# Performance work log

Hardware: AMD Instinct MI355X
Metric: run time of the kernel (lower is better)

Reference implementation:

```python
import jax, jax.numpy as jnp
import numpy as np

N = 100000   # nodes
E = 1600000  # edges
G = 256      # graphs in batch
IN = 128     # in_feats
H = 64       # h_feats


def _xavier(k, shape):
    fan_in, fan_out = shape
    lim = float(np.sqrt(6.0 / (fan_in + fan_out)))
    return jax.random.uniform(k, shape, jnp.float32, -lim, lim)


def setup_inputs() -> dict:
    key = jax.random.key(0)
    ks = jax.random.split(key, 12)
    x = jax.random.normal(ks[0], (N, IN), jnp.float32)
    src = jax.random.randint(ks[1], (E,), 0, N)
    dst = jax.random.randint(ks[2], (E,), 0, N)
    ew = jax.random.uniform(ks[3], (E,), jnp.float32)
    gid = jnp.sort(jax.random.randint(ks[4], (N,), 0, G))
    def lin(k, fi, fo):
        kw, kb = jax.random.split(k)
        lim = float(np.sqrt(1.0 / fi))
        return (jax.random.uniform(kw, (fi, fo), jnp.float32, -lim, lim),
                jax.random.uniform(kb, (fo,), jnp.float32, -lim, lim))
    W1 = _xavier(ks[5], (IN, H)); b1 = jnp.zeros((H,), jnp.float32)
    W2 = _xavier(ks[6], (H, H));  b2 = jnp.zeros((H,), jnp.float32)
    W3 = _xavier(ks[7], (H, H));  b3 = jnp.zeros((H,), jnp.float32)
    Dw1, Db1 = lin(ks[8], H, 16)
    Dw2, Db2 = lin(ks[9], 16, 8)
    Dw3, Db3 = lin(ks[10], 8, 1)
    return {"x": x, "src": src, "dst": dst, "ew": ew, "gid": gid,
            "W1": W1, "b1": b1, "W2": W2, "b2": b2, "W3": W3, "b3": b3,
            "Dw1": Dw1, "Db1": Db1, "Dw2": Dw2, "Db2": Db2, "Dw3": Dw3, "Db3": Db3}


def reference(x, src, dst, ew, gid, W1, b1, W2, b2, W3, b3,
              Dw1, Db1, Dw2, Db2, Dw3, Db3):
    n = x.shape[0]
    # DGL GraphConv norm='both': unweighted degrees, clamped to >= 1
    deg_out = jnp.zeros((n,), x.dtype).at[src].add(1.0)
    deg_in = jnp.zeros((n,), x.dtype).at[dst].add(1.0)
    ns = jax.lax.rsqrt(jnp.maximum(deg_out, 1.0))  # src-side norm
    nd = jax.lax.rsqrt(jnp.maximum(deg_in, 1.0))   # dst-side norm

    def conv(h, W, b):
        # apply weight first (in >= out), then gather-scale-scatter
        h = (h * ns[:, None]) @ W                      # [N, out]
        m = h[src] * ew[:, None]                       # [E, out] edge messages
        agg = jnp.zeros((n, W.shape[1]), h.dtype).at[dst].add(m)
        return agg * nd[:, None] + b

    h = jax.nn.relu(conv(x, W1, b1))
    h = jax.nn.relu(conv(h, W2, b2))
    h = jax.nn.relu(conv(h, W3, b3))

    # mean_nodes: per-graph mean pooling
    counts = jnp.zeros((G,), h.dtype).at[gid].add(1.0)
    pooled = jnp.zeros((G, h.shape[1]), h.dtype).at[gid].add(h)
    pooled = pooled / jnp.maximum(counts, 1.0)[:, None]

    h = jax.nn.relu(pooled @ Dw1 + Db1)
    h = jax.nn.relu(h @ Dw2 + Db2)
    return jax.nn.sigmoid(h @ Dw3 + Db3)  # [G, 1]
```

## Files before the change

### kernel.cpp

```cpp
#include <hip/hip_runtime.h>
#include <math.h>

#define N_NODES 100000
#define N_EDGES 1600000
#define G_GRAPHS 256
#define IN_F 128
#define H_F 64

#define HB 40
#define HCHUNK (N_EDGES / HB)
#define NWORDS (N_NODES / 4)
#define HNODES 25000
#define HWORDS (HNODES / 4)
#define HR 4

#define NREG 160
#define REG_NODES 625
#define BUCKET_CAP 11000
#define BSPAN 6400
#define NB_BUCKET (N_EDGES / BSPAN)

typedef unsigned int uint_t;
typedef unsigned short ushort_t;
typedef unsigned char uchar_t;
typedef __attribute__((ext_vector_type(8))) short short8;
typedef __attribute__((ext_vector_type(4))) float floatx4;
typedef __attribute__((ext_vector_type(2))) float floatx2;

__device__ __forceinline__ ushort_t f2bf(float f) {
  uint_t u = __float_as_uint(f);
  uint_t r = (u + 0x7fffu + ((u >> 16) & 1u)) >> 16;
  return (ushort_t)r;
}
__device__ __forceinline__ float bflo(uint_t u) { return __uint_as_float(u << 16); }
__device__ __forceinline__ uchar_t f2fp8(float f) {
  return (uchar_t)(__builtin_amdgcn_cvt_pk_fp8_f32(f, f, 0, false) & 0xff);
}

__global__ __launch_bounds__(256) void build_a_kernel(
    const int* __restrict__ src, const int* __restrict__ dst,
    const float* __restrict__ ew, int* __restrict__ bcnt,
    uint2* __restrict__ bucket, uint_t* __restrict__ p8src) {
  __shared__ uint_t shm[BSPAN + 2 * NREG];
  if (blockIdx.x < NB_BUCKET) {
    uint_t* rl = shm;
    int* cnt = (int*)(shm + BSPAN);
    int* cur = cnt + NREG;
    const int e0 = blockIdx.x * BSPAN;

    for (int i = threadIdx.x; i < NREG; i += 256) cnt[i] = 0;
    __syncthreads();

    for (int i = threadIdx.x; i < BSPAN; i += 256) {
      uint_t d = (uint_t)dst[e0 + i];
      uint_t r = d / REG_NODES;
      uint_t loc = d - r * REG_NODES;
      rl[i] = (r << 16) | loc;
      atomicAdd(&cnt[r], 1);
    }
    __syncthreads();

    for (int i = threadIdx.x; i < NREG; i += 256)
      cur[i] = atomicAdd(&bcnt[i], cnt[i]);
    __syncthreads();

    for (int i = threadIdx.x; i < BSPAN; i += 256) {
      uint_t v = rl[i];
      uint_t r = v >> 16, loc = v & 0xffffu;
      int pos = atomicAdd(&cur[r], 1);
      if (pos < BUCKET_CAP)
        bucket[(size_t)r * BUCKET_CAP + pos] = make_uint2(
            (loc << 17) | (uint_t)src[e0 + i], __float_as_uint(ew[e0 + i]));
    }
  } else {
    uint_t* h = shm;
    const int idx = blockIdx.x - NB_BUCKET;
    const int r = idx / HB;
    const int b = idx % HB;
    const uint_t rbase = (uint_t)(r * HNODES);

    for (int i = threadIdx.x; i < HWORDS; i += 256) h[i] = 0u;
    __syncthreads();

    const uint4* k4 = (const uint4*)(src + b * HCHUNK);
    for (int i = threadIdx.x; i < HCHUNK / 4; i += 256) {
      uint4 v = k4[i];
      uint_t t;
      t = v.x - rbase; if (t < (uint_t)HNODES) atomicAdd(&h[t >> 2], 1u << ((t & 3u) * 8u));
      t = v.y - rbase; if (t < (uint_t)HNODES) atomicAdd(&h[t >> 2], 1u << ((t & 3u) * 8u));
      t = v.z - rbase; if (t < (uint_t)HNODES) atomicAdd(&h[t >> 2], 1u << ((t & 3u) * 8u));
      t = v.w - rbase; if (t < (uint_t)HNODES) atomicAdd(&h[t >> 2], 1u << ((t & 3u) * 8u));
    }
    __syncthreads();

    uint_t* outp = p8src + (size_t)b * NWORDS + r * HWORDS;
    for (int i = threadIdx.x; i < HWORDS; i += 256) outp[i] = h[i];
  }
}

__global__ __launch_bounds__(256) void build_b_kernel(
    const uint2* __restrict__ bucket, const int* __restrict__ bcnt,
    const uint_t* __restrict__ p8src, uint_t* __restrict__ csr,
    int2* __restrict__ rc, float* __restrict__ nd, float* __restrict__ ns) {
  __shared__ uint_t staged[BUCKET_CAP];
  __shared__ int cnt[REG_NODES];
  __shared__ int sc[REG_NODES];
  __shared__ int ts[256];
  const int tid = threadIdx.x;
  if (blockIdx.x >= NREG) {
    int w = (blockIdx.x - NREG) * 256 + tid;
    if (w >= NWORDS) return;
    int c0 = 0, c1 = 0, c2 = 0, c3 = 0;
    for (int b = 0; b < HB; ++b) {
      uint_t xv = p8src[(size_t)b * NWORDS + w];
      c0 += (int)(xv & 0xffu);
      c1 += (int)((xv >> 8) & 0xffu);
      c2 += (int)((xv >> 16) & 0xffu);
      c3 += (int)((xv >> 24) & 0xffu);
    }
    ((float4*)ns)[w] = make_float4(
        rsqrtf(fmaxf((float)c0, 1.0f)), rsqrtf(fmaxf((float)c1, 1.0f)),
        rsqrtf(fmaxf((float)c2, 1.0f)), rsqrtf(fmaxf((float)c3, 1.0f)));
    return;
  }
  const int r = blockIdx.x;
  const int nE = min(bcnt[r], BUCKET_CAP);

  ts[tid] = (tid < NREG) ? min(bcnt[tid], BUCKET_CAP) : 0;
  for (int i = tid; i < REG_NODES; i += 256) cnt[i] = 0;
  __syncthreads();
  for (int off = 1; off < 256; off <<= 1) {
    int t = (tid >= off) ? ts[tid - off] : 0;
    __syncthreads();
    ts[tid] += t;
    __syncthreads();
  }
  const int csr_base = (r == 0) ? 0 : ts[r - 1];
  __syncthreads();

  const uint2* bk = bucket + (size_t)r * BUCKET_CAP;
  for (int i = tid; i < nE; i += 256) atomicAdd(&cnt[bk[i].x >> 17], 1);
  __syncthreads();

  const int loc0 = tid * 3;
  int c3v[3], s = 0;
#pragma unroll
  for (int k = 0; k < 3; ++k) {
    int idx = loc0 + k;
    c3v[k] = (idx < REG_NODES) ? cnt[idx] : 0;
    s += c3v[k];
  }
  __syncthreads();
  ts[tid] = s;
  __syncthreads();
  for (int off = 1; off < 256; off <<= 1) {
    int t = (tid >= off) ? ts[tid - off] : 0;
    __syncthreads();
    ts[tid] += t;
    __syncthreads();
  }
  int run = (tid == 0) ? 0 : ts[tid - 1];
#pragma unroll
  for (int k = 0; k < 3; ++k) {
    int idx = loc0 + k;
    if (idx < REG_NODES) {
      sc[idx] = run;
      int v = r * REG_NODES + idx;
      rc[v] = make_int2(csr_base + run, c3v[k]);
      nd[v] = rsqrtf(fmaxf((float)c3v[k], 1.0f));
      run += c3v[k];
    }
  }
  __syncthreads();

  for (int i = tid; i < nE; i += 256) {
    uint2 e = bk[i];
    uint_t loc = e.x >> 17;
    int pos = atomicAdd(&sc[loc], 1);
    staged[pos] = ((uint_t)(f2bf(__uint_as_float(e.y)) & 0x7fff) << 17) |
                  (e.x & 0x1ffffu);
  }
  __syncthreads();

  for (int i = tid; i < nE; i += 256) csr[csr_base + i] = staged[i];
}

template <int K, bool AFP32>
__global__ __launch_bounds__(256) void gemm_mfma_kernel(
    const void* __restrict__ Xin, const float* __restrict__ W,
    const float* __restrict__ ns, uchar_t* __restrict__ T, int ntiles) {
  constexpr int CH = K / 32;
  constexpr int WROW = K + 8;
  __shared__ __align__(16) ushort_t Wt[64 * WROW];
  const int tid = threadIdx.x;

  for (int i = tid; i < K * 64; i += 256) {
    int k = i >> 6, nn = i & 63;
    Wt[nn * WROW + k] = f2bf(W[i]);
  }
  __syncthreads();

  const int wave = tid >> 6;
  const int lane = tid & 63;
  const int tile = blockIdx.x * 4 + wave;
  if (tile >= ntiles) return;
  const int m = lane & 15;
  const int q = lane >> 4;
  const int node0 = tile * 16;

  short8 afrag[CH];
  if (AFP32) {
    const float* xr = (const float*)Xin + (size_t)(node0 + m) * K + q * 8;
#pragma unroll
    for (int c = 0; c < CH; ++c) {
      float4 xa = *(const float4*)(xr + c * 32);
      float4 xb = *(const float4*)(xr + c * 32 + 4);
      short8 a;
      a[0] = (short)f2bf(xa.x); a[1] = (short)f2bf(xa.y);
      a[2] = (short)f2bf(xa.z); a[3] = (short)f2bf(xa.w);
      a[4] = (short)f2bf(xb.x); a[5] = (short)f2bf(xb.y);
      a[6] = (short)f2bf(xb.z); a[7] = (short)f2bf(xb.w);
      afrag[c] = a;
    }
  } else {
    const ushort_t* xr = (const ushort_t*)Xin + (size_t)(node0 + m) * K + q * 8;
#pragma unroll
    for (int c = 0; c < CH; ++c)
      afrag[c] = *(const short8*)(xr + c * 32);
  }

  floatx4 acc[4];
#pragma unroll
  for (int t = 0; t < 4; ++t) acc[t] = (floatx4){0.f, 0.f, 0.f, 0.f};

#pragma unroll
  for (int t = 0; t < 4; ++t) {
    const ushort_t* wr = &Wt[(t * 16 + m) * WROW + q * 8];
#pragma unroll
    for (int c = 0; c < CH; ++c) {
      short8 bfrag = *(const short8*)(wr + c * 32);
      acc[t] = __builtin_amdgcn_mfma_f32_16x16x32_bf16(afrag[c], bfrag, acc[t], 0, 0, 0);
    }
  }

  float4 nsv = *(const float4*)(ns + node0 + q * 4);
  const float nsa[4] = {nsv.x, nsv.y, nsv.z, nsv.w};
#pragma unroll
  for (int t = 0; t < 4; ++t) {
#pragma unroll
    for (int r = 0; r < 4; ++r) {
      int node = node0 + q * 4 + r;
      T[(size_t)node * 64 + t * 16 + m] = f2fp8(acc[t][r] * nsa[r]);
    }
  }
}

#define GACC(p, w)                                                   \
  a = __builtin_amdgcn_cvt_pk_f32_fp8((p).x, false);                 \
  acc[0] = fmaf(a.x, (w), acc[0]); acc[1] = fmaf(a.y, (w), acc[1]);  \
  a = __builtin_amdgcn_cvt_pk_f32_fp8((p).x, true);                  \
  acc[2] = fmaf(a.x, (w), acc[2]); acc[3] = fmaf(a.y, (w), acc[3]);  \
  a = __builtin_amdgcn_cvt_pk_f32_fp8((p).y, false);                 \
  acc[4] = fmaf(a.x, (w), acc[4]); acc[5] = fmaf(a.y, (w), acc[5]);  \
  a = __builtin_amdgcn_cvt_pk_f32_fp8((p).y, true);                  \
  acc[6] = fmaf(a.x, (w), acc[6]); acc[7] = fmaf(a.y, (w), acc[7]);

template <bool POOL>
__global__ __launch_bounds__(256) void fused_kernel(
    const uint_t* __restrict__ csr, const int2* __restrict__ rc,
    const uchar_t* __restrict__ T, const float* __restrict__ nd,
    const float* __restrict__ bias, const float* __restrict__ ns,
    const float* __restrict__ W, uchar_t* __restrict__ Tout,
    const int* __restrict__ gid, float* __restrict__ pooled) {
  constexpr int WROW = H_F + 8;
  __shared__ __align__(16) ushort_t Hs[64 * WROW];
  __shared__ __align__(16) ushort_t Wt[64 * WROW];
  __shared__ float gaccF[4 * 64];
  __shared__ int g0s;
  const int tid = threadIdx.x;
  const int node_base = blockIdx.x * 64;

  if constexpr (POOL) {
    gaccF[tid] = 0.0f;
    if (tid == 0) g0s = gid[node_base];
  } else {
    for (int i = tid; i < H_F * 64; i += 256) {
      int k = i >> 6, nn = i & 63;
      Wt[nn * WROW + k] = f2bf(W[i]);
    }
  }
  __syncthreads();

  const int lane = tid & 63;
  const int wv = tid >> 6;
  const int o = lane >> 3, l = lane & 7;

#pragma unroll 1
  for (int pass = 0; pass < 2; ++pass) {
    const int ln = pass * 32 + wv * 8 + o;
    const int v = node_base + ln;
    if (v < N_NODES) {
      int2 rcv = rc[v];
      const int start = rcv.x, cnt = rcv.y;
      float acc[8] = {0, 0, 0, 0, 0, 0, 0, 0};
      floatx2 a;
      int k = 0;
      for (; k + 7 < cnt; k += 8) {
        uint_t e1 = csr[start + k];
        uint_t e2 = csr[start + k + 1];
        uint_t e3 = csr[start + k + 2];
        uint_t e4 = csr[start + k + 3];
        uint_t e5 = csr[start + k + 4];
        uint_t e6 = csr[start + k + 5];
        uint_t e7 = csr[start + k + 6];
        uint_t e8 = csr[start + k + 7];
        uint2 p1 = *((const uint2*)(T + (size_t)(e1 & 0x1ffffu) * 64) + l);
        uint2 p2 = *((const uint2*)(T + (size_t)(e2 & 0x1ffffu) * 64) + l);
        uint2 p3 = *((const uint2*)(T + (size_t)(e3 & 0x1ffffu) * 64) + l);
        uint2 p4 = *((const uint2*)(T + (size_t)(e4 & 0x1ffffu) * 64) + l);
        uint2 p5 = *((const uint2*)(T + (size_t)(e5 & 0x1ffffu) * 64) + l);
        uint2 p6 = *((const uint2*)(T + (size_t)(e6 & 0x1ffffu) * 64) + l);
        uint2 p7 = *((const uint2*)(T + (size_t)(e7 & 0x1ffffu) * 64) + l);
        uint2 p8 = *((const uint2*)(T + (size_t)(e8 & 0x1ffffu) * 64) + l);
        float w1 = __uint_as_float((e1 >> 17) << 16);
        float w2 = __uint_as_float((e2 >> 17) << 16);
        float w3 = __uint_as_float((e3 >> 17) << 16);
        float w4 = __uint_as_float((e4 >> 17) << 16);
        float w5 = __uint_as_float((e5 >> 17) << 16);
        float w6 = __uint_as_float((e6 >> 17) << 16);
        float w7 = __uint_as_float((e7 >> 17) << 16);
        float w8 = __uint_as_float((e8 >> 17) << 16);
        GACC(p1, w1) GACC(p2, w2) GACC(p3, w3) GACC(p4, w4)
        GACC(p5, w5) GACC(p6, w6) GACC(p7, w7) GACC(p8, w8)
      }
      for (; k + 3 < cnt; k += 4) {
        uint_t e1 = csr[start + k];
        uint_t e2 = csr[start + k + 1];
        uint_t e3 = csr[start + k + 2];
        uint_t e4 = csr[start + k + 3];
        uint2 p1 = *((const uint2*)(T + (size_t)(e1 & 0x1ffffu) * 64) + l);
        uint2 p2 = *((const uint2*)(T + (size_t)(e2 & 0x1ffffu) * 64) + l);
        uint2 p3 = *((const uint2*)(T + (size_t)(e3 & 0x1ffffu) * 64) + l);
        uint2 p4 = *((const uint2*)(T + (size_t)(e4 & 0x1ffffu) * 64) + l);
        float w1 = __uint_as_float((e1 >> 17) << 16);
        float w2 = __uint_as_float((e2 >> 17) << 16);
        float w3 = __uint_as_float((e3 >> 17) << 16);
        float w4 = __uint_as_float((e4 >> 17) << 16);
        GACC(p1, w1) GACC(p2, w2) GACC(p3, w3) GACC(p4, w4)
      }
      for (; k < cnt; ++k) {
        uint_t e1 = csr[start + k];
        float w1 = __uint_as_float((e1 >> 17) << 16);
        uint2 p1 = *((const uint2*)(T + (size_t)(e1 & 0x1ffffu) * 64) + l);
        GACC(p1, w1)
      }

      const float ndv = nd[v];
      float4 b0 = *(const float4*)&bias[l * 8];
      float4 b1v = *(const float4*)&bias[l * 8 + 4];
      if constexpr (!POOL) {
        uint4 ov;
        ov.x = (uint_t)f2bf(fmaxf(fmaf(acc[0], ndv, b0.x), 0.f)) |
               ((uint_t)f2bf(fmaxf(fmaf(acc[1], ndv, b0.y), 0.f)) << 16);
        ov.y = (uint_t)f2bf(fmaxf(fmaf(acc[2], ndv, b0.z), 0.f)) |
               ((uint_t)f2bf(fmaxf(fmaf(acc[3], ndv, b0.w), 0.f)) << 16);
        ov.z = (uint_t)f2bf(fmaxf(fmaf(acc[4], ndv, b1v.x), 0.f)) |
               ((uint_t)f2bf(fmaxf(fmaf(acc[5], ndv, b1v.y), 0.f)) << 16);
        ov.w = (uint_t)f2bf(fmaxf(fmaf(acc[6], ndv, b1v.z), 0.f)) |
               ((uint_t)f2bf(fmaxf(fmaf(acc[7], ndv, b1v.w), 0.f)) << 16);
        *((uint4*)&Hs[ln * WROW + l * 8]) = ov;
      } else {
        const float bb[8] = {b0.x, b0.y, b0.z, b0.w, b1v.x, b1v.y, b1v.z, b1v.w};
        float vals[8];
#pragma unroll
        for (int f = 0; f < 8; ++f)
          vals[f] = bflo((uint_t)f2bf(fmaxf(fmaf(acc[f], ndv, bb[f]), 0.f)));
        int g = gid[v];
        int gl = g - g0s;
        if (gl >= 0 && gl < 4) {
#pragma unroll
          for (int f = 0; f < 8; ++f)
            atomicAdd(&gaccF[gl * 64 + l * 8 + f], vals[f]);
        } else {
#pragma unroll
          for (int f = 0; f < 8; ++f)
            atomicAdd(&pooled[(size_t)g * 64 + l * 8 + f], vals[f]);
        }
      }
    }
  }
  __syncthreads();

  if constexpr (!POOL) {
    const int m = lane & 15, q = lane >> 4;
    const int node0 = node_base + wv * 16;
    if (node0 < N_NODES) {
      short8 afrag[2];
      const ushort_t* xr = &Hs[(wv * 16 + m) * WROW + q * 8];
      afrag[0] = *(const short8*)(xr);
      afrag[1] = *(const short8*)(xr + 32);

      floatx4 acc4[4];
#pragma unroll
      for (int t = 0; t < 4; ++t) acc4[t] = (floatx4){0.f, 0.f, 0.f, 0.f};
#pragma unroll
      for (int t = 0; t < 4; ++t) {
        const ushort_t* wr = &Wt[(t * 16 + m) * WROW + q * 8];
#pragma unroll
        for (int c = 0; c < 2; ++c) {
          short8 bfrag = *(const short8*)(wr + c * 32);
          acc4[t] = __builtin_amdgcn_mfma_f32_16x16x32_bf16(afrag[c], bfrag,
                                                           acc4[t], 0, 0, 0);
        }
      }
      float4 nsv = *(const float4*)(ns + node0 + q * 4);
      const float nsa[4] = {nsv.x, nsv.y, nsv.z, nsv.w};
#pragma unroll
      for (int t = 0; t < 4; ++t) {
#pragma unroll
        for (int r2 = 0; r2 < 4; ++r2) {
          int node = node0 + q * 4 + r2;
          Tout[(size_t)node * 64 + t * 16 + m] = f2fp8(acc4[t][r2] * nsa[r2]);
        }
      }
    }
  } else {
    int vlast = node_base + 63;
    if (vlast >= N_NODES) vlast = N_NODES - 1;
    int span = gid[vlast] - g0s + 1;
    if (span > 4) span = 4;
    if (tid < span * 64) {
      int gl = tid >> 6, j = tid & 63;
      int g = g0s + gl;
      if (g < G_GRAPHS) {
        float vsum = gaccF[gl * 64 + j];
        if (vsum != 0.0f) atomicAdd(&pooled[(size_t)g * 64 + j], vsum);
      }
    }
  }
}

__global__ __launch_bounds__(256) void pool_mlp_kernel(
    const float* __restrict__ pooled, const int* __restrict__ gid,
    const float* __restrict__ Dw1, const float* __restrict__ Db1,
    const float* __restrict__ Dw2, const float* __restrict__ Db2,
    const float* __restrict__ Dw3, const float* __restrict__ Db3,
    float* __restrict__ out) {
  __shared__ float mean[64];
  __shared__ float h1s[16], h2s[8];
  const int g = blockIdx.x;
  int l = 0, r = N_NODES;
  while (l < r) { int m = (l + r) >> 1; if (gid[m] < g) l = m + 1; else r = m; }
  const int lo = l;
  r = N_NODES;
  while (l < r) { int m = (l + r) >> 1; if (gid[m] < g + 1) l = m + 1; else r = m; }
  const int hi = l;

  if (threadIdx.x < 64) {
    float inv = 1.0f / fmaxf((float)(hi - lo), 1.0f);
    mean[threadIdx.x] = pooled[(size_t)g * 64 + threadIdx.x] * inv;
  }
  __syncthreads();
  if (threadIdx.x < 16) {
    int o = threadIdx.x;
    float a = Db1[o];
#pragma unroll
    for (int k = 0; k < 64; ++k) a = fmaf(mean[k], Dw1[k * 16 + o], a);
    h1s[o] = fmaxf(a, 0.0f);
  }
  __syncthreads();
  if (threadIdx.x < 8) {
    int o = threadIdx.x;
    float a = Db2[o];
#pragma unroll
    for (int k = 0; k < 16; ++k) a = fmaf(h1s[k], Dw2[k * 8 + o], a);
    h2s[o] = fmaxf(a, 0.0f);
  }
  __syncthreads();
  if (threadIdx.x == 0) {
    float a = Db3[0];
#pragma unroll
    for (int k = 0; k < 8; ++k) a = fmaf(h2s[k], Dw3[k], a);
    out[g] = 1.0f / (1.0f + expf(-a));
  }
}

extern "C" void kernel_launch(void* const* d_in, const int* in_sizes, int n_in,
                              void* d_out, int out_size, void* d_ws, size_t ws_size,
                              hipStream_t stream) {
  const float* x   = (const float*)d_in[0];
  const int*   src = (const int*)  d_in[1];
  const int*   dst = (const int*)  d_in[2];
  const float* ew  = (const float*)d_in[3];
  const int*   gid = (const int*)  d_in[4];
  const float* W1  = (const float*)d_in[5];
  const float* b1  = (const float*)d_in[6];
  const float* W2  = (const float*)d_in[7];
  const float* b2  = (const float*)d_in[8];
  const float* W3  = (const float*)d_in[9];
  const float* b3  = (const float*)d_in[10];
  const float* Dw1 = (const float*)d_in[11];
  const float* Db1 = (const float*)d_in[12];
  const float* Dw2 = (const float*)d_in[13];
  const float* Db2 = (const float*)d_in[14];
  const float* Dw3 = (const float*)d_in[15];
  const float* Db3 = (const float*)d_in[16];
  float* out = (float*)d_out;

  char* ws = (char*)d_ws;
  const size_t TSZ = (size_t)N_NODES * 64;
  const size_t BUCKET_BYTES = (size_t)NREG * BUCKET_CAP * 8;
  uchar_t*  T_a   = (uchar_t*)ws;
  uchar_t*  T_b   = (uchar_t*)(ws + TSZ);
  uint2*    bucket = (uint2*)ws;
  char* p = ws + BUCKET_BYTES;
  uint_t*   csr   = (uint_t*)p;          p += (size_t)N_EDGES * 4;
  uint_t*   p8src = (uint_t*)p;          p += (size_t)HB * NWORDS * 4;
  float*    ns    = (float*)p;           p += (size_t)N_NODES * 4;
  float*    nd    = (float*)p;           p += (size_t)N_NODES * 4;
  int2*     rc    = (int2*)p;            p += (size_t)N_NODES * 8;
  int*      bcnt  = (int*)p;             p += (size_t)NREG * 4;
  float*    pooled = (float*)p;

  const int NTILES  = N_NODES / 16;
  const int NB_A    = NB_BUCKET + HR * HB;
  const int NB_B    = NREG + (NWORDS + 255) / 256;
  const int NB_GEMM = (NTILES + 3) / 4;
  const int NB_F    = (N_NODES + 63) / 64;

  hipMemsetAsync(bcnt, 0,
                 NREG * sizeof(int) + G_GRAPHS * H_F * sizeof(float), stream);
  build_a_kernel<<<NB_A, 256, 0, stream>>>(src, dst, ew, bcnt, bucket, p8src);
  build_b_kernel<<<NB_B, 256, 0, stream>>>(bucket, bcnt, p8src, csr, rc, nd, ns);

  gemm_mfma_kernel<IN_F, true><<<NB_GEMM, 256, 0, stream>>>(x, W1, ns, T_a, NTILES);
  fused_kernel<false><<<NB_F, 256, 0, stream>>>(csr, rc, T_a, nd, b1, ns, W2,
                                                T_b, nullptr, nullptr);
  fused_kernel<false><<<NB_F, 256, 0, stream>>>(csr, rc, T_b, nd, b2, ns, W3,
                                                T_a, nullptr, nullptr);
  fused_kernel<true><<<NB_F, 256, 0, stream>>>(csr, rc, T_a, nd, b3, nullptr,
                                               nullptr, nullptr, gid, pooled);

  pool_mlp_kernel<<<G_GRAPHS, 256, 0, stream>>>(pooled, gid, Dw1, Db1, Dw2, Db2,
                                                Dw3, Db3, out);
}
```

Measured before the change: 295.4 us.

## Interleave two nodes' gathers per thread and widen CSR build blocks

The SpMM aggregation loop now processes the two nodes each thread owns at the same time, issuing eight-edge gather batches for both before accumulating. This doubles the number of independent loads in flight to hide gather latency, and the fused kernel gets a launch-bounds occupancy hint of 4. Separately, build_b uses 1024-thread blocks, so each thread scans one region node instead of three and the scan runs over 1024 entries. The costs are higher register pressure in the fused kernel and more barrier steps in the wider scan.

```diff
diff --git a/kernel.cpp b/kernel.cpp
--- a/kernel.cpp
+++ b/kernel.cpp
@@ -26,6 +26,8 @@
 typedef __attribute__((ext_vector_type(8))) short short8;
 typedef __attribute__((ext_vector_type(4))) float floatx4;
 typedef __attribute__((ext_vector_type(2))) float floatx2;
+
+constexpr int WROW_F = H_F + 8;
 
 __device__ __forceinline__ ushort_t f2bf(float f) {
   uint_t u = __float_as_uint(f);
@@ -98,17 +100,17 @@
   }
 }
 
-__global__ __launch_bounds__(256) void build_b_kernel(
+__global__ __launch_bounds__(1024) void build_b_kernel(
     const uint2* __restrict__ bucket, const int* __restrict__ bcnt,
     const uint_t* __restrict__ p8src, uint_t* __restrict__ csr,
     int2* __restrict__ rc, float* __restrict__ nd, float* __restrict__ ns) {
   __shared__ uint_t staged[BUCKET_CAP];
   __shared__ int cnt[REG_NODES];
   __shared__ int sc[REG_NODES];
-  __shared__ int ts[256];
+  __shared__ int ts[1024];
   const int tid = threadIdx.x;
   if (blockIdx.x >= NREG) {
-    int w = (blockIdx.x - NREG) * 256 + tid;
+    int w = (blockIdx.x - NREG) * 1024 + tid;
     if (w >= NWORDS) return;
     int c0 = 0, c1 = 0, c2 = 0, c3 = 0;
     for (int b = 0; b < HB; ++b) {
@@ -127,7 +129,7 @@
   const int nE = min(bcnt[r], BUCKET_CAP);
 
   ts[tid] = (tid < NREG) ? min(bcnt[tid], BUCKET_CAP) : 0;
-  for (int i = tid; i < REG_NODES; i += 256) cnt[i] = 0;
+  for (int i = tid; i < REG_NODES; i += 1024) cnt[i] = 0;
   __syncthreads();
   for (int off = 1; off < 256; off <<= 1) {
     int t = (tid >= off) ? ts[tid - off] : 0;
@@ -139,41 +141,28 @@
   __syncthreads();
 
   const uint2* bk = bucket + (size_t)r * BUCKET_CAP;
-  for (int i = tid; i < nE; i += 256) atomicAdd(&cnt[bk[i].x >> 17], 1);
-  __syncthreads();
-
-  const int loc0 = tid * 3;
-  int c3v[3], s = 0;
-#pragma unroll
-  for (int k = 0; k < 3; ++k) {
-    int idx = loc0 + k;
-    c3v[k] = (idx < REG_NODES) ? cnt[idx] : 0;
-    s += c3v[k];
-  }
-  __syncthreads();
-  ts[tid] = s;
-  __syncthreads();
-  for (int off = 1; off < 256; off <<= 1) {
+  for (int i = tid; i < nE; i += 1024) atomicAdd(&cnt[bk[i].x >> 17], 1);
+  __syncthreads();
+
+  int cv = (tid < REG_NODES) ? cnt[tid] : 0;
+  ts[tid] = cv;
+  __syncthreads();
+  for (int off = 1; off < 1024; off <<= 1) {
     int t = (tid >= off) ? ts[tid - off] : 0;
     __syncthreads();
     ts[tid] += t;
     __syncthreads();
   }
-  int run = (tid == 0) ? 0 : ts[tid - 1];
-#pragma unroll
-  for (int k = 0; k < 3; ++k) {
-    int idx = loc0 + k;
-    if (idx < REG_NODES) {
-      sc[idx] = run;
-      int v = r * REG_NODES + idx;
-      rc[v] = make_int2(csr_base + run, c3v[k]);
-      nd[v] = rsqrtf(fmaxf((float)c3v[k], 1.0f));
-      run += c3v[k];
-    }
-  }
-  __syncthreads();
-
-  for (int i = tid; i < nE; i += 256) {
+  if (tid < REG_NODES) {
+    int run = (tid == 0) ? 0 : ts[tid - 1];
+    sc[tid] = run;
+    int v = r * REG_NODES + tid;
+    rc[v] = make_int2(csr_base + run, cv);
+    nd[v] = rsqrtf(fmaxf((float)cv, 1.0f));
+  }
+  __syncthreads();
+
+  for (int i = tid; i < nE; i += 1024) {
     uint2 e = bk[i];
     uint_t loc = e.x >> 17;
     int pos = atomicAdd(&sc[loc], 1);
@@ -182,7 +171,7 @@
   }
   __syncthreads();
 
-  for (int i = tid; i < nE; i += 256) csr[csr_base + i] = staged[i];
+  for (int i = tid; i < nE; i += 1024) csr[csr_base + i] = staged[i];
 }
 
 template <int K, bool AFP32>
@@ -255,26 +244,95 @@
   }
 }
 
-#define GACC(p, w)                                                   \
-  a = __builtin_amdgcn_cvt_pk_f32_fp8((p).x, false);                 \
-  acc[0] = fmaf(a.x, (w), acc[0]); acc[1] = fmaf(a.y, (w), acc[1]);  \
-  a = __builtin_amdgcn_cvt_pk_f32_fp8((p).x, true);                  \
-  acc[2] = fmaf(a.x, (w), acc[2]); acc[3] = fmaf(a.y, (w), acc[3]);  \
-  a = __builtin_amdgcn_cvt_pk_f32_fp8((p).y, false);                 \
-  acc[4] = fmaf(a.x, (w), acc[4]); acc[5] = fmaf(a.y, (w), acc[5]);  \
-  a = __builtin_amdgcn_cvt_pk_f32_fp8((p).y, true);                  \
-  acc[6] = fmaf(a.x, (w), acc[6]); acc[7] = fmaf(a.y, (w), acc[7]);
+__device__ __forceinline__ void ld_e8(const uint_t* __restrict__ c, int k,
+                                      uint_t e[8]) {
+#pragma unroll
+  for (int j = 0; j < 8; ++j) e[j] = c[k + j];
+}
+__device__ __forceinline__ void ld_p8(const uchar_t* __restrict__ T, int l,
+                                      const uint_t e[8], uint2 p[8]) {
+#pragma unroll
+  for (int j = 0; j < 8; ++j)
+    p[j] = *((const uint2*)(T + (size_t)(e[j] & 0x1ffffu) * 64) + l);
+}
+__device__ __forceinline__ void gacc1(float acc[8], uint_t e, uint2 p) {
+  float w = __uint_as_float((e >> 17) << 16);
+  floatx2 a;
+  a = __builtin_amdgcn_cvt_pk_f32_fp8(p.x, false);
+  acc[0] = fmaf(a.x, w, acc[0]); acc[1] = fmaf(a.y, w, acc[1]);
+  a = __builtin_amdgcn_cvt_pk_f32_fp8(p.x, true);
+  acc[2] = fmaf(a.x, w, acc[2]); acc[3] = fmaf(a.y, w, acc[3]);
+  a = __builtin_amdgcn_cvt_pk_f32_fp8(p.y, false);
+  acc[4] = fmaf(a.x, w, acc[4]); acc[5] = fmaf(a.y, w, acc[5]);
+  a = __builtin_amdgcn_cvt_pk_f32_fp8(p.y, true);
+  acc[6] = fmaf(a.x, w, acc[6]); acc[7] = fmaf(a.y, w, acc[7]);
+}
+__device__ __forceinline__ void gacc8(float acc[8], const uint_t e[8],
+                                      const uint2 p[8]) {
+#pragma unroll
+  for (int j = 0; j < 8; ++j) gacc1(acc, e[j], p[j]);
+}
+__device__ __forceinline__ void ld_e4(const uint_t* __restrict__ c, int k,
+                                      uint_t e[4]) {
+#pragma unroll
+  for (int j = 0; j < 4; ++j) e[j] = c[k + j];
+}
+__device__ __forceinline__ void ld_p4(const uchar_t* __restrict__ T, int l,
+                                      const uint_t e[4], uint2 p[4]) {
+#pragma unroll
+  for (int j = 0; j < 4; ++j)
+    p[j] = *((const uint2*)(T + (size_t)(e[j] & 0x1ffffu) * 64) + l);
+}
+__device__ __forceinline__ void gacc4(float acc[8], const uint_t e[4],
+                                      const uint2 p[4]) {
+#pragma unroll
+  for (int j = 0; j < 4; ++j) gacc1(acc, e[j], p[j]);
+}
+
+__device__ __forceinline__ void hs_store(ushort_t* Hs, int row, int l,
+                                         const float acc[8], float ndv,
+                                         float4 b0, float4 b1v) {
+  uint4 ov;
+  ov.x = (uint_t)f2bf(fmaxf(fmaf(acc[0], ndv, b0.x), 0.f)) |
+         ((uint_t)f2bf(fmaxf(fmaf(acc[1], ndv, b0.y), 0.f)) << 16);
+  ov.y = (uint_t)f2bf(fmaxf(fmaf(acc[2], ndv, b0.z), 0.f)) |
+         ((uint_t)f2bf(fmaxf(fmaf(acc[3], ndv, b0.w), 0.f)) << 16);
+  ov.z = (uint_t)f2bf(fmaxf(fmaf(acc[4], ndv, b1v.x), 0.f)) |
+         ((uint_t)f2bf(fmaxf(fmaf(acc[5], ndv, b1v.y), 0.f)) << 16);
+  ov.w = (uint_t)f2bf(fmaxf(fmaf(acc[6], ndv, b1v.z), 0.f)) |
+         ((uint_t)f2bf(fmaxf(fmaf(acc[7], ndv, b1v.w), 0.f)) << 16);
+  *((uint4*)&Hs[row * WROW_F + l * 8]) = ov;
+}
+
+__device__ __forceinline__ void pool_acc(float* gaccF, float* pooled, int g,
+                                         int g0s, int l, const float acc[8],
+                                         float ndv, float4 b0, float4 b1v) {
+  const float bb[8] = {b0.x, b0.y, b0.z, b0.w, b1v.x, b1v.y, b1v.z, b1v.w};
+  float vals[8];
+#pragma unroll
+  for (int f = 0; f < 8; ++f)
+    vals[f] = bflo((uint_t)f2bf(fmaxf(fmaf(acc[f], ndv, bb[f]), 0.f)));
+  int gl = g - g0s;
+  if (gl >= 0 && gl < 4) {
+#pragma unroll
+    for (int f = 0; f < 8; ++f)
+      atomicAdd(&gaccF[gl * 64 + l * 8 + f], vals[f]);
+  } else {
+#pragma unroll
+    for (int f = 0; f < 8; ++f)
+      atomicAdd(&pooled[(size_t)g * 64 + l * 8 + f], vals[f]);
+  }
+}
 
 template <bool POOL>
-__global__ __launch_bounds__(256) void fused_kernel(
+__global__ __launch_bounds__(256, 4) void fused_kernel(
     const uint_t* __restrict__ csr, const int2* __restrict__ rc,
     const uchar_t* __restrict__ T, const float* __restrict__ nd,
     const float* __restrict__ bias, const float* __restrict__ ns,
     const float* __restrict__ W, uchar_t* __restrict__ Tout,
     const int* __restrict__ gid, float* __restrict__ pooled) {
-  constexpr int WROW = H_F + 8;
-  __shared__ __align__(16) ushort_t Hs[64 * WROW];
-  __shared__ __align__(16) ushort_t Wt[64 * WROW];
+  __shared__ __align__(16) ushort_t Hs[64 * WROW_F];
+  __shared__ __align__(16) ushort_t Wt[64 * WROW_F];
   __shared__ float gaccF[4 * 64];
   __shared__ int g0s;
   const int tid = threadIdx.x;
@@ -286,7 +344,7 @@
   } else {
     for (int i = tid; i < H_F * 64; i += 256) {
       int k = i >> 6, nn = i & 63;
-      Wt[nn * WROW + k] = f2bf(W[i]);
+      Wt[nn * WROW_F + k] = f2bf(W[i]);
     }
   }
   __syncthreads();
@@ -295,99 +353,72 @@
   const int wv = tid >> 6;
   const int o = lane >> 3, l = lane & 7;
 
-#pragma unroll 1
-  for (int pass = 0; pass < 2; ++pass) {
-    const int ln = pass * 32 + wv * 8 + o;
-    const int v = node_base + ln;
-    if (v < N_NODES) {
-      int2 rcv = rc[v];
-      const int start = rcv.x, cnt = rcv.y;
-      float acc[8] = {0, 0, 0, 0, 0, 0, 0, 0};
-      floatx2 a;
-      int k = 0;
-      for (; k + 7 < cnt; k += 8) {
-        uint_t e1 = csr[start + k];
-        uint_t e2 = csr[start + k + 1];
-        uint_t e3 = csr[start + k + 2];
-        uint_t e4 = csr[start + k + 3];
-        uint_t e5 = csr[start + k + 4];
-        uint_t e6 = csr[start + k + 5];
-        uint_t e7 = csr[start + k + 6];
-        uint_t e8 = csr[start + k + 7];
-        uint2 p1 = *((const uint2*)(T + (size_t)(e1 & 0x1ffffu) * 64) + l);
-        uint2 p2 = *((const uint2*)(T + (size_t)(e2 & 0x1ffffu) * 64) + l);
-        uint2 p3 = *((const uint2*)(T + (size_t)(e3 & 0x1ffffu) * 64) + l);
-        uint2 p4 = *((const uint2*)(T + (size_t)(e4 & 0x1ffffu) * 64) + l);
-        uint2 p5 = *((const uint2*)(T + (size_t)(e5 & 0x1ffffu) * 64) + l);
-        uint2 p6 = *((const uint2*)(T + (size_t)(e6 & 0x1ffffu) * 64) + l);
-        uint2 p7 = *((const uint2*)(T + (size_t)(e7 & 0x1ffffu) * 64) + l);
-        uint2 p8 = *((const uint2*)(T + (size_t)(e8 & 0x1ffffu) * 64) + l);
-        float w1 = __uint_as_float((e1 >> 17) << 16);
-        float w2 = __uint_as_float((e2 >> 17) << 16);
-        float w3 = __uint_as_float((e3 >> 17) << 16);
-        float w4 = __uint_as_float((e4 >> 17) << 16);
-        float w5 = __uint_as_float((e5 >> 17) << 16);
-        float w6 = __uint_as_float((e6 >> 17) << 16);
-        float w7 = __uint_as_float((e7 >> 17) << 16);
-        float w8 = __uint_as_float((e8 >> 17) << 16);
-        GACC(p1, w1) GACC(p2, w2) GACC(p3, w3) GACC(p4, w4)
-        GACC(p5, w5) GACC(p6, w6) GACC(p7, w7) GACC(p8, w8)
-      }
-      for (; k + 3 < cnt; k += 4) {
-        uint_t e1 = csr[start + k];
-        uint_t e2 = csr[start + k + 1];
-        uint_t e3 = csr[start + k + 2];
-        uint_t e4 = csr[start + k + 3];
-        uint2 p1 = *((const uint2*)(T + (size_t)(e1 & 0x1ffffu) * 64) + l);
-        uint2 p2 = *((const uint2*)(T + (size_t)(e2 & 0x1ffffu) * 64) + l);
-        uint2 p3 = *((const uint2*)(T + (size_t)(e3 & 0x1ffffu) * 64) + l);
-        uint2 p4 = *((const uint2*)(T + (size_t)(e4 & 0x1ffffu) * 64) + l);
-        float w1 = __uint_as_float((e1 >> 17) << 16);
-        float w2 = __uint_as_float((e2 >> 17) << 16);
-        float w3 = __uint_as_float((e3 >> 17) << 16);
-        float w4 = __uint_as_float((e4 >> 17) << 16);
-        GACC(p1, w1) GACC(p2, w2) GACC(p3, w3) GACC(p4, w4)
-      }
-      for (; k < cnt; ++k) {
-        uint_t e1 = csr[start + k];
-        float w1 = __uint_as_float((e1 >> 17) << 16);
-        uint2 p1 = *((const uint2*)(T + (size_t)(e1 & 0x1ffffu) * 64) + l);
-        GACC(p1, w1)
-      }
-
-      const float ndv = nd[v];
-      float4 b0 = *(const float4*)&bias[l * 8];
-      float4 b1v = *(const float4*)&bias[l * 8 + 4];
-      if constexpr (!POOL) {
-        uint4 ov;
-        ov.x = (uint_t)f2bf(fmaxf(fmaf(acc[0], ndv, b0.x), 0.f)) |
-               ((uint_t)f2bf(fmaxf(fmaf(acc[1], ndv, b0.y), 0.f)) << 16);
-        ov.y = (uint_t)f2bf(fmaxf(fmaf(acc[2], ndv, b0.z), 0.f)) |
-               ((uint_t)f2bf(fmaxf(fmaf(acc[3], ndv, b0.w), 0.f)) << 16);
-        ov.z = (uint_t)f2bf(fmaxf(fmaf(acc[4], ndv, b1v.x), 0.f)) |
-               ((uint_t)f2bf(fmaxf(fmaf(acc[5], ndv, b1v.y), 0.f)) << 16);
-        ov.w = (uint_t)f2bf(fmaxf(fmaf(acc[6], ndv, b1v.z), 0.f)) |
-               ((uint_t)f2bf(fmaxf(fmaf(acc[7], ndv, b1v.w), 0.f)) << 16);
-        *((uint4*)&Hs[ln * WROW + l * 8]) = ov;
-      } else {
-        const float bb[8] = {b0.x, b0.y, b0.z, b0.w, b1v.x, b1v.y, b1v.z, b1v.w};
-        float vals[8];
-#pragma unroll
-        for (int f = 0; f < 8; ++f)
-          vals[f] = bflo((uint_t)f2bf(fmaxf(fmaf(acc[f], ndv, bb[f]), 0.f)));
-        int g = gid[v];
-        int gl = g - g0s;
-        if (gl >= 0 && gl < 4) {
-#pragma unroll
-          for (int f = 0; f < 8; ++f)
-            atomicAdd(&gaccF[gl * 64 + l * 8 + f], vals[f]);
-        } else {
-#pragma unroll
-          for (int f = 0; f < 8; ++f)
-            atomicAdd(&pooled[(size_t)g * 64 + l * 8 + f], vals[f]);
-        }
-      }
-    }
+  const int ln = wv * 8 + o;
+  const int vA = node_base + ln;
+  const int vB = vA + 32;
+  const bool bok = (vB < N_NODES);
+
+  int2 rcA = rc[vA];
+  int2 rcB = bok ? rc[vB] : make_int2(0, 0);
+  const uint_t* cA = csr + rcA.x;
+  const uint_t* cB = csr + rcB.x;
+  const int cntA = rcA.y, cntB = rcB.y;
+
+  float accA[8] = {0, 0, 0, 0, 0, 0, 0, 0};
+  float accB[8] = {0, 0, 0, 0, 0, 0, 0, 0};
+  int kA = 0, kB = 0;
+
+  while ((kA + 8 <= cntA) && (kB + 8 <= cntB)) {
+    uint_t eA[8], eB[8];
+    uint2 pA[8], pB[8];
+    ld_e8(cA, kA, eA);
+    ld_e8(cB, kB, eB);
+    ld_p8(T, l, eA, pA);
+    ld_p8(T, l, eB, pB);
+    gacc8(accA, eA, pA);
+    gacc8(accB, eB, pB);
+    kA += 8;
+    kB += 8;
+  }
+  while (kA + 8 <= cntA) {
+    uint_t e[8]; uint2 p[8];
+    ld_e8(cA, kA, e); ld_p8(T, l, e, p); gacc8(accA, e, p); kA += 8;
+  }
+  while (kB + 8 <= cntB) {
+    uint_t e[8]; uint2 p[8];
+    ld_e8(cB, kB, e); ld_p8(T, l, e, p); gacc8(accB, e, p); kB += 8;
+  }
+  {
+    const bool a4 = (kA + 4 <= cntA), b4 = (kB + 4 <= cntB);
+    uint_t e4a[4], e4b[4];
+    uint2 p4a[4], p4b[4];
+    if (a4) { ld_e4(cA, kA, e4a); ld_p4(T, l, e4a, p4a); }
+    if (b4) { ld_e4(cB, kB, e4b); ld_p4(T, l, e4b, p4b); }
+    if (a4) { gacc4(accA, e4a, p4a); kA += 4; }
+    if (b4) { gacc4(accB, e4b, p4b); kB += 4; }
+  }
+  for (; kA < cntA; ++kA) {
+    uint_t e = cA[kA];
+    uint2 p = *((const uint2*)(T + (size_t)(e & 0x1ffffu) * 64) + l);
+    gacc1(accA, e, p);
+  }
+  for (; kB < cntB; ++kB) {
+    uint_t e = cB[kB];
+    uint2 p = *((const uint2*)(T + (size_t)(e & 0x1ffffu) * 64) + l);
+    gacc1(accB, e, p);
+  }
+
+  const float4 b0 = *(const float4*)&bias[l * 8];
+  const float4 b1v = *(const float4*)&bias[l * 8 + 4];
+  const float ndA = nd[vA];
+  const float ndB = bok ? nd[vB] : 0.0f;
+
+  if constexpr (!POOL) {
+    hs_store(Hs, ln, l, accA, ndA, b0, b1v);
+    if (bok) hs_store(Hs, ln + 32, l, accB, ndB, b0, b1v);
+  } else {
+    pool_acc(gaccF, pooled, gid[vA], g0s, l, accA, ndA, b0, b1v);
+    if (bok) pool_acc(gaccF, pooled, gid[vB], g0s, l, accB, ndB, b0, b1v);
   }
   __syncthreads();
 
@@ -396,21 +427,21 @@
     const int node0 = node_base + wv * 16;
     if (node0 < N_NODES) {
       short8 afrag[2];
-      const ushort_t* xr = &Hs[(wv * 16 + m) * WROW + q * 8];
+      const ushort_t* xr = &Hs[(wv * 16 + m) * WROW_F + q * 8];
       afrag[0] = *(const short8*)(xr);
       afrag[1] = *(const short8*)(xr + 32);
 
-      floatx4 acc4[4];
-#pragma unroll
-      for (int t = 0; t < 4; ++t) acc4[t] = (floatx4){0.f, 0.f, 0.f, 0.f};
+      floatx4 acc4v[4];
+#pragma unroll
+      for (int t = 0; t < 4; ++t) acc4v[t] = (floatx4){0.f, 0.f, 0.f, 0.f};
 #pragma unroll
       for (int t = 0; t < 4; ++t) {
-        const ushort_t* wr = &Wt[(t * 16 + m) * WROW + q * 8];
+        const ushort_t* wr = &Wt[(t * 16 + m) * WROW_F + q * 8];
 #pragma unroll
         for (int c = 0; c < 2; ++c) {
           short8 bfrag = *(const short8*)(wr + c * 32);
-          acc4[t] = __builtin_amdgcn_mfma_f32_16x16x32_bf16(afrag[c], bfrag,
-                                                           acc4[t], 0, 0, 0);
+          acc4v[t] = __builtin_amdgcn_mfma_f32_16x16x32_bf16(afrag[c], bfrag,
+                                                            acc4v[t], 0, 0, 0);
         }
       }
       float4 nsv = *(const float4*)(ns + node0 + q * 4);
@@ -420,7 +451,7 @@
 #pragma unroll
         for (int r2 = 0; r2 < 4; ++r2) {
           int node = node0 + q * 4 + r2;
-          Tout[(size_t)node * 64 + t * 16 + m] = f2fp8(acc4[t][r2] * nsa[r2]);
+          Tout[(size_t)node * 64 + t * 16 + m] = f2fp8(acc4v[t][r2] * nsa[r2]);
         }
       }
     }
@@ -524,14 +555,14 @@
 
   const int NTILES  = N_NODES / 16;
   const int NB_A    = NB_BUCKET + HR * HB;
-  const int NB_B    = NREG + (NWORDS + 255) / 256;
+  const int NB_B    = NREG + (NWORDS + 1023) / 1024;
   const int NB_GEMM = (NTILES + 3) / 4;
   const int NB_F    = (N_NODES + 63) / 64;
 
   hipMemsetAsync(bcnt, 0,
                  NREG * sizeof(int) + G_GRAPHS * H_F * sizeof(float), stream);
   build_a_kernel<<<NB_A, 256, 0, stream>>>(src, dst, ew, bcnt, bucket, p8src);
-  build_b_kernel<<<NB_B, 256, 0, stream>>>(bucket, bcnt, p8src, csr, rc, nd, ns);
+  build_b_kernel<<<NB_B, 1024, 0, stream>>>(bucket, bcnt, p8src, csr, rc, nd, ns);
 
   gemm_mfma_kernel<IN_F, true><<<NB_GEMM, 256, 0, stream>>>(x, W1, ns, T_a, NTILES);
   fused_kernel<false><<<NB_F, 256, 0, stream>>>(csr, rc, T_a, nd, b1, ns, W2,
```

After: 304.3 us. 3.0% more time.
